# Performance work log

Measured on AMD Instinct MI355X. Metric: run time of the kernel, lower is better.

## Reference

```python
import jax, jax.numpy as jnp
import numpy as np

N, C, H, W = 512, 512, 7, 7
K = 64
ALPHA = 100.0
HW = H * W


def _up13(x):
    # bilinear upsample (..., 7, 7) -> (..., 13, 13), align_corners=True
    src = jnp.arange(13, dtype=jnp.float32) * (6.0 / 12.0)
    i0 = jnp.floor(src).astype(jnp.int32)
    i1 = jnp.minimum(i0 + 1, 6)
    w = src - i0.astype(jnp.float32)
    xr = x[..., i0, :] * (1.0 - w)[:, None] + x[..., i1, :] * w[:, None]  # rows
    xc = xr[..., :, i0] * (1.0 - w) + xr[..., :, i1] * w                  # cols
    return xc


def _conv2d(x, w, b, p):
    y = jax.lax.conv_general_dilated(
        x, w, window_strides=(1, 1), padding=[(p, p), (p, p)],
        dimension_numbers=('NCHW', 'OIHW', 'NCHW'))
    return y + b[None, :, None, None]


def setup_inputs() -> dict:
    key = jax.random.key(0)
    ks = jax.random.split(key, 16)
    x = jax.random.normal(ks[0], (N, C, H, W), jnp.float32)
    centroids = jax.random.uniform(ks[1], (K, C), jnp.float32)
    # conv params initialized from centroids as in _init_params (separate params after init)
    conv_w = 2.0 * ALPHA * centroids                    # (K, C) 1x1 conv kernel
    conv_b = -ALPHA * jnp.linalg.norm(centroids, axis=1)
    ln_w = jnp.ones((7, 7), jnp.float32)
    ln_b = jnp.zeros((7, 7), jnp.float32)
    c3_w = 0.02 * jax.random.normal(ks[2], (32, 512, 3, 3), jnp.float32)
    c3_b = jnp.zeros((32,), jnp.float32)
    c5_w = 0.02 * jax.random.normal(ks[3], (32, 512, 5, 5), jnp.float32)
    c5_b = jnp.zeros((32,), jnp.float32)
    c7_w = 0.02 * jax.random.normal(ks[4], (20, 512, 7, 7), jnp.float32)
    c7_b = jnp.zeros((20,), jnp.float32)
    dw_w = 0.1 * jax.random.normal(ks[5], (7, 13), jnp.float32)
    dw_b = jnp.zeros((7,), jnp.float32)
    dh_w = 0.1 * jax.random.normal(ks[6], (7, 13), jnp.float32)
    dh_b = jnp.zeros((7,), jnp.float32)
    acc_w = 0.1 * jax.random.normal(ks[7], (1, 84), jnp.float32)  # 1x1 conv (O, I)
    acc_b = jnp.zeros((1,), jnp.float32)
    return dict(x=x, centroids=centroids, conv_w=conv_w, conv_b=conv_b,
                ln_w=ln_w, ln_b=ln_b, c3_w=c3_w, c3_b=c3_b, c5_w=c5_w, c5_b=c5_b,
                c7_w=c7_w, c7_b=c7_b, dw_w=dw_w, dw_b=dw_b, dh_w=dh_w, dh_b=dh_b,
                acc_w=acc_w, acc_b=acc_b)


def reference(x, centroids, conv_w, conv_b, ln_w, ln_b,
              c3_w, c3_b, c5_w, c5_b, c7_w, c7_b,
              dw_w, dw_b, dh_w, dh_b, acc_w, acc_b):
    # ---- CRN on the raw (un-normalized) input ----
    mu = jnp.mean(x, axis=(-2, -1), keepdims=True)
    var = jnp.mean((x - mu) ** 2, axis=(-2, -1), keepdims=True)
    h = (x - mu) / jnp.sqrt(var + 1e-5) * ln_w + ln_b          # LayerNorm([7,7])
    h = _up13(h)                                               # (N,512,13,13)
    h = jnp.concatenate([_conv2d(h, c3_w, c3_b, 1),
                         _conv2d(h, c5_w, c5_b, 2),
                         _conv2d(h, c7_w, c7_b, 3)], axis=1)   # (N,84,13,13)
    h = jnp.einsum('nchw,ow->ncho', h, dw_w) + dw_b            # width 13->7
    h = h.transpose(0, 1, 3, 2)
    h = jnp.einsum('nchw,ow->ncho', h, dh_w) + dh_b            # height 13->7
    cw = jnp.einsum('nchw,oc->nohw', h, acc_w) + acc_b[None, :, None, None]
    cw = cw.reshape(N, 1, HW)                                  # context weights

    # ---- descriptor-wise L2 normalization over channels ----
    nrm = jnp.sqrt(jnp.sum(x * x, axis=1, keepdims=True))
    xn = x / jnp.maximum(nrm, 1e-12)

    # ---- soft assignment (1x1 conv + softmax over clusters) ----
    logits = (jnp.einsum('nchw,kc->nkhw', xn, conv_w)
              + conv_b[None, :, None, None]).reshape(N, K, HW)
    sa = jax.nn.softmax(logits, axis=1)
    mask = sa * cw                                             # (N,K,HW)

    # ---- fused VLAD aggregation (same math as masked residual sum) ----
    xf = xn.reshape(N, C, HW)
    vlad = jnp.einsum('nkl,ncl->nkc', mask, xf) \
        - centroids[None, :, :] * jnp.sum(mask, axis=-1)[:, :, None]
    vlad = vlad / jnp.maximum(jnp.linalg.norm(vlad, axis=2, keepdims=True), 1e-12)
    vlad = vlad.reshape(N, K * C)
    vlad = vlad / jnp.maximum(jnp.linalg.norm(vlad, axis=1, keepdims=True), 1e-12)
    return vlad
```

## Files before the change

kernel.cpp:

```cpp
#include <hip/hip_runtime.h>
#include <math.h>

#define NI 512
#define CC 512
#define KCL 64
#define HW49 49
#define CQ 25088
#define AP 260
#define GP 68
#define XQP 132

__device__ __forceinline__ float Uval(int i, int u) {
    if (i & 1) return (u == ((i - 1) >> 1) || u == ((i + 1) >> 1)) ? 0.5f : 0.0f;
    return (u == (i >> 1)) ? 1.0f : 0.0f;
}

__global__ __launch_bounds__(256) void kG(
    const float* __restrict__ c3w, const float* __restrict__ c5w, const float* __restrict__ c7w,
    const float* __restrict__ dww, const float* __restrict__ dhw, const float* __restrict__ accw,
    const float* __restrict__ lnw, const float* __restrict__ lnb,
    float* __restrict__ Gmat, float* __restrict__ Gl)
{
    const int c = blockIdx.x;
    const int t = threadIdx.x;
    __shared__ float dh[91], dw[91];
    __shared__ float Fh3[147], Fw3[147], Fh5[245], Fw5[245], Fh7[343], Fw7[343];
    __shared__ float wa3[9], wa5[25], wa7[49];
    __shared__ float Gtmp[2401];
    if (t < 91) dh[t] = dhw[t];
    if (t >= 128 && t < 219) dw[t - 128] = dww[t - 128];
    __syncthreads();
    for (int idx = t; idx < 147; idx += 256) {
        int oh = idx / 21, r = idx % 21, u = r / 3, dy = r % 3;
        float sh = 0.f, sw = 0.f;
        for (int i = 0; i < 13; i++) { int y = i - dy + 1; if (y >= 0 && y < 13) { float uu = Uval(i, u); sh += dh[oh * 13 + y] * uu; sw += dw[oh * 13 + y] * uu; } }
        Fh3[idx] = sh; Fw3[idx] = sw;
    }
    for (int idx = t; idx < 245; idx += 256) {
        int oh = idx / 35, r = idx % 35, u = r / 5, dy = r % 5;
        float sh = 0.f, sw = 0.f;
        for (int i = 0; i < 13; i++) { int y = i - dy + 2; if (y >= 0 && y < 13) { float uu = Uval(i, u); sh += dh[oh * 13 + y] * uu; sw += dw[oh * 13 + y] * uu; } }
        Fh5[idx] = sh; Fw5[idx] = sw;
    }
    for (int idx = t; idx < 343; idx += 256) {
        int oh = idx / 49, r = idx % 49, u = r / 7, dy = r % 7;
        float sh = 0.f, sw = 0.f;
        for (int i = 0; i < 13; i++) { int y = i - dy + 3; if (y >= 0 && y < 13) { float uu = Uval(i, u); sh += dh[oh * 13 + y] * uu; sw += dw[oh * 13 + y] * uu; } }
        Fh7[idx] = sh; Fw7[idx] = sw;
    }
    if (t < 9)               { float s = 0.f; for (int co = 0; co < 32; co++) s += accw[co]      * c3w[(size_t)(co * 512 + c) * 9  + t];        wa3[t] = s; }
    if (t >= 32 && t < 57)   { int q = t - 32; float s = 0.f; for (int co = 0; co < 32; co++) s += accw[32 + co] * c5w[(size_t)(co * 512 + c) * 25 + q]; wa5[q] = s; }
    if (t >= 64 && t < 113)  { int q = t - 64; float s = 0.f; for (int co = 0; co < 20; co++) s += accw[64 + co] * c7w[(size_t)(co * 512 + c) * 49 + q]; wa7[q] = s; }
    __syncthreads();
    for (int o = t; o < 2401; o += 256) {
        int q = o / 49, p = o % 49;
        int u = q / 7, v = q % 7, ow = p / 7, oh = p % 7;
        float acc = 0.f;
        #pragma unroll
        for (int dy = 0; dy < 3; dy++) { float fh = Fh3[(oh * 7 + u) * 3 + dy];
            #pragma unroll
            for (int dx = 0; dx < 3; dx++) acc += wa3[dy * 3 + dx] * fh * Fw3[(ow * 7 + v) * 3 + dx]; }
        #pragma unroll
        for (int dy = 0; dy < 5; dy++) { float fh = Fh5[(oh * 7 + u) * 5 + dy];
            #pragma unroll
            for (int dx = 0; dx < 5; dx++) acc += wa5[dy * 5 + dx] * fh * Fw5[(ow * 7 + v) * 5 + dx]; }
        #pragma unroll
        for (int dy = 0; dy < 7; dy++) { float fh = Fh7[(oh * 7 + u) * 7 + dy];
            #pragma unroll
            for (int dx = 0; dx < 7; dx++) acc += wa7[dy * 7 + dx] * fh * Fw7[(ow * 7 + v) * 7 + dx]; }
        Gtmp[o] = acc;
        Gmat[(size_t)c * 2401 + o] = acc * lnw[q];
    }
    __syncthreads();
    if (t < 49) {
        float s = 0.f;
        for (int q = 0; q < 49; q++) s += Gtmp[q * 49 + t] * lnb[q];
        Gl[c * 49 + t] = s;
    }
}

__global__ void kCb(const float* __restrict__ c3b, const float* __restrict__ c5b, const float* __restrict__ c7b,
                    const float* __restrict__ dww, const float* __restrict__ dwb,
                    const float* __restrict__ dhw, const float* __restrict__ dhb,
                    const float* __restrict__ accw, const float* __restrict__ accb,
                    const float* __restrict__ Gl, float* __restrict__ Cb)
{
    __shared__ float A0s, A1s, Sdw[7], Sdh[7];
    int t = threadIdx.x;
    if (t == 0) {
        float a0 = 0.f, a1 = 0.f;
        for (int co = 0; co < 84; co++) {
            float aw = accw[co]; a0 += aw;
            float b = (co < 32) ? c3b[co] : ((co < 64) ? c5b[co - 32] : c7b[co - 64]);
            a1 += aw * b;
        }
        A0s = a0; A1s = a1;
    }
    if (t < 7)             { float s = 0.f; for (int xx = 0; xx < 13; xx++) s += dww[t * 13 + xx]; Sdw[t] = s; }
    if (t >= 8 && t < 15)  { int oh = t - 8; float s = 0.f; for (int y = 0; y < 13; y++) s += dhw[oh * 13 + y]; Sdh[oh] = s; }
    __syncthreads();
    if (t < 49) {
        int ow = t / 7, oh = t % 7;
        float g = 0.f;
        for (int c = 0; c < 512; c++) g += Gl[c * 49 + t];
        Cb[t] = A1s * Sdw[ow] * Sdh[oh] + A0s * (dwb[ow] * Sdh[oh] + dhb[oh]) + accb[0] + g;
    }
}

__global__ __launch_bounds__(512) void kCw1(const float* __restrict__ x,
    const float* __restrict__ Gmat, float* __restrict__ part)
{
    __shared__ float As[49 * AP];
    __shared__ float Gs[49 * GP];
    const int b = blockIdx.x;
    const int nt = b >> 8, ks = b & 255;
    const int n0 = nt * 256;
    const int t = threadIdx.x;
    const int tn = t >> 3;
    const int tp = t & 7;
    float acc[4][8];
    #pragma unroll
    for (int j = 0; j < 4; j++)
        #pragma unroll
        for (int m = 0; m < 8; m++) acc[j][m] = 0.f;
    for (int kk = 0; kk < 2; kk++) {
        const int c = ks * 2 + kk;
        for (int i = t; i < 12544; i += 512) {
            int nr = i / 49, q = i - nr * 49;
            As[q * AP + nr] = x[(size_t)(n0 + nr) * CQ + (size_t)c * 49 + q];
        }
        for (int i = t; i < 2401; i += 512) {
            int q = i / 49, p = i - q * 49;
            Gs[q * GP + p] = Gmat[(size_t)c * 2401 + i];
        }
        for (int i = t; i < 735; i += 512) {
            int q = i / 15, pc = 49 + (i - q * 15);
            Gs[q * GP + pc] = 0.f;
        }
        __syncthreads();
        if (t < 256) {
            float s = 0.f, ss = 0.f;
            for (int q = 0; q < 49; q++) { float v = As[q * AP + t]; s += v; ss += v * v; }
            float mu = s * (1.f / 49.f);
            float var = ss * (1.f / 49.f) - mu * mu;
            float rs = 1.f / sqrtf(var + 1e-5f);
            for (int q = 0; q < 49; q++) As[q * AP + t] = (As[q * AP + t] - mu) * rs;
        }
        __syncthreads();
        for (int q = 0; q < 49; q++) {
            float4 a0 = *(const float4*)&As[q * AP + tn * 4];
            float4 g0 = *(const float4*)&Gs[q * GP + tp * 8];
            float4 g1 = *(const float4*)&Gs[q * GP + tp * 8 + 4];
            float av[4] = {a0.x, a0.y, a0.z, a0.w};
            float gv[8] = {g0.x, g0.y, g0.z, g0.w, g1.x, g1.y, g1.z, g1.w};
            #pragma unroll
            for (int j = 0; j < 4; j++)
                #pragma unroll
                for (int m = 0; m < 8; m++) acc[j][m] += av[j] * gv[m];
        }
        __syncthreads();
    }
    #pragma unroll
    for (int j = 0; j < 4; j++) {
        #pragma unroll
        for (int m = 0; m < 8; m++) {
            int p = tp * 8 + m;
            if (p < 49) As[(tn * 4 + j) * 49 + p] = acc[j][m];
        }
    }
    __syncthreads();
    {
        float* dst = part + (size_t)ks * CQ + (size_t)n0 * 49;
        for (int i = t; i < 12544; i += 512) dst[i] = As[i];
    }
}

__global__ __launch_bounds__(512) void kLog(const float* __restrict__ x,
    const float* __restrict__ convw, const float* __restrict__ convb,
    const float* __restrict__ part, const float* __restrict__ Cbg,
    float* __restrict__ maskr, float* __restrict__ msum)
{
    __shared__ float xq[2][49 * XQP];
    __shared__ float lg[64 * 52];
    __shared__ float ps[8 * 56];
    __shared__ float rn[49], cwl[49], smax[49], sinv[49];
    __shared__ float cb[64];
    __shared__ float pmx[392], psm[392];
    const int n = blockIdx.x;
    const int t = threadIdx.x;
    const int lane = t & 63;
    const int kw = __builtin_amdgcn_readfirstlane(t >> 6);
    const float* xp = x + (size_t)n * CQ;

    int scg[4], sl[4];
    #pragma unroll
    for (int s = 0; s < 4; s++) {
        int idx = t + s * 512;
        scg[s] = idx / 49; sl[s] = idx - scg[s] * 49;
    }
    float4 r[4];
    #pragma unroll
    for (int s = 0; s < 4; s++) {
        if (s < 3 || t < 32) {
            const float* src = xp + (size_t)(scg[s] * 4) * 49 + sl[s];
            r[s].x = src[0]; r[s].y = src[49]; r[s].z = src[98]; r[s].w = src[147];
        }
    }
    if (lane < 49) {
        const float* bp = part + (size_t)(kw * 32) * CQ + (size_t)n * 49 + lane;
        float s0 = 0.f, s1 = 0.f, s2 = 0.f, s3 = 0.f;
        for (int i = 0; i < 32; i += 4) {
            s0 += bp[(size_t)(i + 0) * CQ];
            s1 += bp[(size_t)(i + 1) * CQ];
            s2 += bp[(size_t)(i + 2) * CQ];
            s3 += bp[(size_t)(i + 3) * CQ];
        }
        psm[lane * 8 + kw] = (s0 + s1) + (s2 + s3);
    }
    if (t < 64) cb[t] = convb[t];

    float a[8] = {0.f, 0.f, 0.f, 0.f, 0.f, 0.f, 0.f, 0.f};
    float rs_part = 0.f;

    #pragma unroll
    for (int s = 0; s < 4; s++)
        if (s < 3 || t < 32) *(float4*)&xq[0][sl[s] * XQP + scg[s] * 4] = r[s];
    #pragma unroll
    for (int s = 0; s < 4; s++) {
        if (s < 3 || t < 32) {
            const float* src = xp + (size_t)(128 + scg[s] * 4) * 49 + sl[s];
            r[s].x = src[0]; r[s].y = src[49]; r[s].z = src[98]; r[s].w = src[147];
        }
    }
    __syncthreads();
    if (t < 49) {
        float s = Cbg[t];
        #pragma unroll
        for (int q = 0; q < 8; q++) s += psm[t * 8 + q];
        cwl[t] = s;
    }
    for (int qt = 0; qt < 4; qt++) {
        const float* buf = xq[qt & 1];
        if (lane < 49) {
            const float* row = &buf[lane * XQP + kw * 16];
            #pragma unroll
            for (int c4 = 0; c4 < 4; c4++) {
                float4 v = *(const float4*)(row + c4 * 4);
                rs_part += v.x * v.x + v.y * v.y + v.z * v.z + v.w * v.w;
            }
        }
        {
            const int lr = (lane < 49) ? lane : 48;
            const float* xrow = &buf[lr * XQP];
            const float* wb = convw + (size_t)(kw * 8) * 512 + qt * 128;
            for (int c4 = 0; c4 < 32; c4++) {
                float4 xv = *(const float4*)(xrow + c4 * 4);
                #pragma unroll
                for (int j = 0; j < 8; j++) {
                    float4 wv = *(const float4*)&wb[j * 512 + c4 * 4];
                    a[j] += wv.x * xv.x + wv.y * xv.y + wv.z * xv.z + wv.w * xv.w;
                }
            }
        }
        if (qt < 3) {
            #pragma unroll
            for (int s = 0; s < 4; s++)
                if (s < 3 || t < 32) *(float4*)&xq[(qt + 1) & 1][sl[s] * XQP + scg[s] * 4] = r[s];
            if (qt < 2) {
                #pragma unroll
                for (int s = 0; s < 4; s++) {
                    if (s < 3 || t < 32) {
                        const float* src = xp + (size_t)((qt + 2) * 128 + scg[s] * 4) * 49 + sl[s];
                        r[s].x = src[0]; r[s].y = src[49]; r[s].z = src[98]; r[s].w = src[147];
                    }
                }
            }
            __syncthreads();
        }
    }
    if (lane < 49) ps[kw * 56 + lane] = rs_part;
    __syncthreads();
    if (t < 49) {
        float s = 0.f;
        #pragma unroll
        for (int q = 0; q < 8; q++) s += ps[q * 56 + t];
        rn[t] = 1.f / fmaxf(sqrtf(s), 1e-12f);
    }
    __syncthreads();
    if (lane < 49) {
        float r0 = rn[lane];
        #pragma unroll
        for (int j = 0; j < 8; j++) lg[(kw * 8 + j) * 52 + lane] = a[j] * r0 + cb[kw * 8 + j];
    }
    __syncthreads();
    if (t < 392) {
        int l = t >> 3, kq = t & 7;
        float m = -3.402823466e38f;
        #pragma unroll
        for (int j = 0; j < 8; j++) m = fmaxf(m, lg[(kq * 8 + j) * 52 + l]);
        pmx[t] = m;
    }
    __syncthreads();
    if (t < 49) {
        float m = pmx[t * 8];
        #pragma unroll
        for (int q = 1; q < 8; q++) m = fmaxf(m, pmx[t * 8 + q]);
        smax[t] = m;
    }
    __syncthreads();
    if (t < 392) {
        int l = t >> 3, kq = t & 7;
        float m = smax[l], s = 0.f;
        #pragma unroll
        for (int j = 0; j < 8; j++) s += __expf(lg[(kq * 8 + j) * 52 + l] - m);
        psm[t] = s;
    }
    __syncthreads();
    if (t < 49) {
        float s = 0.f;
        #pragma unroll
        for (int q = 0; q < 8; q++) s += psm[t * 8 + q];
        sinv[t] = 1.f / s;
    }
    __syncthreads();
    if (t < 392) {
        int l = t >> 3, kq = t & 7;
        float m = smax[l], si = sinv[l] * cwl[l];
        #pragma unroll
        for (int j = 0; j < 8; j++) {
            int idx = (kq * 8 + j) * 52 + l;
            lg[idx] = __expf(lg[idx] - m) * si;
        }
    }
    __syncthreads();
    {
        float msr[8];
        #pragma unroll
        for (int j = 0; j < 8; j++) {
            float s = 0.f;
            for (int l = 0; l < 49; l++) s += lg[(kw * 8 + j) * 52 + l];
            msr[j] = s;
        }
        if (lane == 0) {
            #pragma unroll
            for (int j = 0; j < 8; j++) msum[n * 64 + kw * 8 + j] = msr[j];
        }
    }
    for (int o = t; o < 3136; o += 512) {
        int k = o / 49, l = o - k * 49;
        maskr[(size_t)n * 3136 + o] = lg[k * 52 + l] * rn[l];
    }
}

__global__ __launch_bounds__(512) void kVd(const float* __restrict__ x,
    const float* __restrict__ maskr, const float* __restrict__ msum,
    const float* __restrict__ cent, float* __restrict__ out)
{
    __shared__ float xh[12560];
    __shared__ float lg[64 * 52];
    __shared__ float ssq[64], scl[64];
    const int n = blockIdx.x;
    const int t = threadIdx.x;
    const int lane = t & 63;
    const int kw = __builtin_amdgcn_readfirstlane(t >> 6);
    const float* xp = x + (size_t)n * CQ;
    for (int i = t; i < 3136; i += 512) { int k = i / 49, l = i - k * 49; lg[k * 52 + l] = maskr[(size_t)n * 3136 + i]; }
    for (int i = t; i < 192; i += 512) { lg[(i / 3) * 52 + 49 + (i % 3)] = 0.f; }
    float msr[8];
    #pragma unroll
    for (int j = 0; j < 8; j++) msr[j] = msum[n * 64 + kw * 8 + j];
    float accA[8][4], accB[8][4];
    #pragma unroll
    for (int j = 0; j < 8; j++)
        #pragma unroll
        for (int ci = 0; ci < 4; ci++) { accA[j][ci] = 0.f; accB[j][ci] = 0.f; }
    for (int i4 = t; i4 < 3136; i4 += 512)
        *(float4*)&xh[i4 * 4] = *(const float4*)&xp[12544 + i4 * 4];
    if (t < 16) xh[12544 + t] = 0.f;
    __syncthreads();
    for (int lq = 0; lq < 13; lq++) {
        float xr[4][4];
        #pragma unroll
        for (int ci = 0; ci < 4; ci++)
            #pragma unroll
            for (int dl = 0; dl < 4; dl++)
                xr[ci][dl] = xh[(lane + 64 * ci) * 49 + lq * 4 + dl];
        #pragma unroll
        for (int j = 0; j < 8; j++) {
            float4 mv = *(const float4*)&lg[(kw * 8 + j) * 52 + lq * 4];
            #pragma unroll
            for (int ci = 0; ci < 4; ci++)
                accB[j][ci] += mv.x * xr[ci][0] + mv.y * xr[ci][1] + mv.z * xr[ci][2] + mv.w * xr[ci][3];
        }
    }
    __syncthreads();
    for (int i4 = t; i4 < 3136; i4 += 512)
        *(float4*)&xh[i4 * 4] = *(const float4*)&xp[i4 * 4];
    if (t < 16) xh[12544 + t] = 0.f;
    __syncthreads();
    for (int lq = 0; lq < 13; lq++) {
        float xr[4][4];
        #pragma unroll
        for (int ci = 0; ci < 4; ci++)
            #pragma unroll
            for (int dl = 0; dl < 4; dl++)
                xr[ci][dl] = xh[(lane + 64 * ci) * 49 + lq * 4 + dl];
        #pragma unroll
        for (int j = 0; j < 8; j++) {
            float4 mv = *(const float4*)&lg[(kw * 8 + j) * 52 + lq * 4];
            #pragma unroll
            for (int ci = 0; ci < 4; ci++)
                accA[j][ci] += mv.x * xr[ci][0] + mv.y * xr[ci][1] + mv.z * xr[ci][2] + mv.w * xr[ci][3];
        }
    }
    float ssr[8];
    #pragma unroll
    for (int j = 0; j < 8; j++) {
        int k = kw * 8 + j;
        float ms = msr[j];
        float s = 0.f;
        #pragma unroll
        for (int ci = 0; ci < 4; ci++) {
            int c = lane + 64 * ci;
            float va = accA[j][ci] - cent[(size_t)k * 512 + c] * ms;
            float vb = accB[j][ci] - cent[(size_t)k * 512 + 256 + c] * ms;
            accA[j][ci] = va; accB[j][ci] = vb;
            s += va * va + vb * vb;
        }
        ssr[j] = s;
    }
    #pragma unroll
    for (int j = 0; j < 8; j++)
        for (int off = 32; off >= 1; off >>= 1) ssr[j] += __shfl_xor(ssr[j], off, 64);
    if (lane == 0) {
        #pragma unroll
        for (int j = 0; j < 8; j++) ssq[kw * 8 + j] = ssr[j];
    }
    __syncthreads();
    if (t < 64) {
        float nrm = sqrtf(ssq[t]);
        float inv = 1.f / fmaxf(nrm, 1e-12f);
        float sk = nrm * inv;
        float g = sk * sk;
        #pragma unroll
        for (int off = 32; off >= 1; off >>= 1) g += __shfl_xor(g, off, 64);
        scl[t] = inv * (1.f / fmaxf(sqrtf(g), 1e-12f));
    }
    __syncthreads();
    #pragma unroll
    for (int j = 0; j < 8; j++) {
        int k = kw * 8 + j;
        float s2 = scl[k];
        #pragma unroll
        for (int ci = 0; ci < 4; ci++) {
            int c = lane + 64 * ci;
            out[(size_t)n * 32768 + (size_t)k * 512 + c] = accA[j][ci] * s2;
            out[(size_t)n * 32768 + (size_t)k * 512 + 256 + c] = accB[j][ci] * s2;
        }
    }
}

extern "C" void kernel_launch(void* const* d_in, const int* in_sizes, int n_in,
                              void* d_out, int out_size, void* d_ws, size_t ws_size,
                              hipStream_t stream)
{
    const float* x     = (const float*)d_in[0];
    const float* cent  = (const float*)d_in[1];
    const float* convw = (const float*)d_in[2];
    const float* convb = (const float*)d_in[3];
    const float* lnw   = (const float*)d_in[4];
    const float* lnb   = (const float*)d_in[5];
    const float* c3w   = (const float*)d_in[6];
    const float* c3b   = (const float*)d_in[7];
    const float* c5w   = (const float*)d_in[8];
    const float* c5b   = (const float*)d_in[9];
    const float* c7w   = (const float*)d_in[10];
    const float* c7b   = (const float*)d_in[11];
    const float* dww   = (const float*)d_in[12];
    const float* dwb   = (const float*)d_in[13];
    const float* dhw   = (const float*)d_in[14];
    const float* dhb   = (const float*)d_in[15];
    const float* accw  = (const float*)d_in[16];
    const float* accb  = (const float*)d_in[17];
    float* out = (float*)d_out;

    char* ws = (char*)d_ws;
    float* Gmat  = (float*)(ws);
    float* Gl    = (float*)(ws + 4917248);
    float* Cb    = (float*)(ws + 5017600);
    float* part  = (float*)(ws + 5017856);
    float* maskr = (float*)(ws + 30707968);
    float* msumW = (float*)(ws + 37130496);

    kG   <<<512, 256, 0, stream>>>(c3w, c5w, c7w, dww, dhw, accw, lnw, lnb, Gmat, Gl);
    kCb  <<<1,   64,  0, stream>>>(c3b, c5b, c7b, dww, dwb, dhw, dhb, accw, accb, Gl, Cb);
    kCw1 <<<512, 512, 0, stream>>>(x, Gmat, part);
    kLog <<<512, 512, 0, stream>>>(x, convw, convb, part, Cb, maskr, msumW);
    kVd  <<<512, 512, 0, stream>>>(x, maskr, msumW, cent, out);
}
```

Baseline: 180.9 us.

## Split logits kernel into channel-halved partial GEMM and separate softmax kernel

The fused logits/softmax kernel is split in two. The first kernel runs 1024 blocks, each computing partial logits and squared norms over half of the channels for one sample. The second kernel sums the two partials, normalizes, and does the softmax and masking. This doubles the block count to raise occupancy and shrinks shared memory per block, at the cost of an extra launch and a global round trip for the partial logits.

After: 283.4 us. 56.6% more time.

```diff
diff --git a/kernel.cpp b/kernel.cpp
--- a/kernel.cpp
+++ b/kernel.cpp
@@ -8,7 +8,7 @@
 #define CQ 25088
 #define AP 260
 #define GP 68
-#define XQP 132
+#define EP 68
 
 __device__ __forceinline__ float Uval(int i, int u) {
     if (i & 1) return (u == ((i - 1) >> 1) || u == ((i + 1) >> 1)) ? 0.5f : 0.0f;
@@ -175,14 +175,102 @@
     }
 }
 
-__global__ __launch_bounds__(512) void kLog(const float* __restrict__ x,
-    const float* __restrict__ convw, const float* __restrict__ convb,
-    const float* __restrict__ part, const float* __restrict__ Cbg,
-    float* __restrict__ maskr, float* __restrict__ msum)
-{
-    __shared__ float xq[2][49 * XQP];
+__global__ __launch_bounds__(512) void kLogA(const float* __restrict__ x,
+    const float* __restrict__ convw, float* __restrict__ lgP, float* __restrict__ rnP)
+{
+    __shared__ float xq[2][49 * EP];
+    __shared__ float ps[8 * 56];
+    const int b = blockIdx.x;
+    const int n = b >> 1, h = b & 1;
+    const int t = threadIdx.x;
+    const int lane = t & 63;
+    const int kw = __builtin_amdgcn_readfirstlane(t >> 6);
+    const float* xp = x + (size_t)n * CQ + (size_t)h * 12544;
+
+    int scg[2], sl[2];
+    #pragma unroll
+    for (int s = 0; s < 2; s++) { int idx = t + s * 512; scg[s] = idx / 49; sl[s] = idx - scg[s] * 49; }
+    const bool v1 = (t < 272);
+    float4 r[2];
+    #pragma unroll
+    for (int s = 0; s < 2; s++) {
+        if (s == 0 || v1) {
+            const float* src = xp + (size_t)(scg[s] * 4) * 49 + sl[s];
+            r[s].x = src[0]; r[s].y = src[49]; r[s].z = src[98]; r[s].w = src[147];
+        }
+    }
+    #pragma unroll
+    for (int s = 0; s < 2; s++)
+        if (s == 0 || v1) *(float4*)&xq[0][sl[s] * EP + scg[s] * 4] = r[s];
+    #pragma unroll
+    for (int s = 0; s < 2; s++) {
+        if (s == 0 || v1) {
+            const float* src = xp + 3136 + (size_t)(scg[s] * 4) * 49 + sl[s];
+            r[s].x = src[0]; r[s].y = src[49]; r[s].z = src[98]; r[s].w = src[147];
+        }
+    }
+    __syncthreads();
+
+    float a[8] = {0.f, 0.f, 0.f, 0.f, 0.f, 0.f, 0.f, 0.f};
+    float rs_part = 0.f;
+    for (int e = 0; e < 4; e++) {
+        const float* buf = xq[e & 1];
+        if (lane < 49) {
+            const float* row = &buf[lane * EP + kw * 8];
+            float4 v0 = *(const float4*)(row);
+            float4 v4 = *(const float4*)(row + 4);
+            rs_part += v0.x * v0.x + v0.y * v0.y + v0.z * v0.z + v0.w * v0.w
+                     + v4.x * v4.x + v4.y * v4.y + v4.z * v4.z + v4.w * v4.w;
+        }
+        {
+            const int lr = (lane < 49) ? lane : 48;
+            const float* xrow = &buf[lr * EP];
+            const float* wb = convw + (size_t)(kw * 8) * 512 + h * 256 + e * 64;
+            for (int c4 = 0; c4 < 16; c4++) {
+                float4 xv = *(const float4*)(xrow + c4 * 4);
+                #pragma unroll
+                for (int j = 0; j < 8; j++) {
+                    float4 wv = *(const float4*)&wb[(size_t)j * 512 + c4 * 4];
+                    a[j] += wv.x * xv.x + wv.y * xv.y + wv.z * xv.z + wv.w * xv.w;
+                }
+            }
+        }
+        if (e < 3) {
+            #pragma unroll
+            for (int s = 0; s < 2; s++)
+                if (s == 0 || v1) *(float4*)&xq[(e + 1) & 1][sl[s] * EP + scg[s] * 4] = r[s];
+            if (e < 2) {
+                #pragma unroll
+                for (int s = 0; s < 2; s++) {
+                    if (s == 0 || v1) {
+                        const float* src = xp + (size_t)(e + 2) * 3136 + (size_t)(scg[s] * 4) * 49 + sl[s];
+                        r[s].x = src[0]; r[s].y = src[49]; r[s].z = src[98]; r[s].w = src[147];
+                    }
+                }
+            }
+            __syncthreads();
+        }
+    }
+    if (lane < 49) ps[kw * 56 + lane] = rs_part;
+    __syncthreads();
+    if (t < 49) {
+        float s = 0.f;
+        #pragma unroll
+        for (int q = 0; q < 8; q++) s += ps[q * 56 + t];
+        rnP[(size_t)(n * 2 + h) * 49 + t] = s;
+    }
+    if (lane < 49) {
+        float* dst = lgP + (size_t)(n * 2 + h) * 3136;
+        #pragma unroll
+        for (int j = 0; j < 8; j++) dst[(kw * 8 + j) * 49 + lane] = a[j];
+    }
+}
+
+__global__ __launch_bounds__(512) void kSoft(const float* __restrict__ lgP,
+    const float* __restrict__ rnP, const float* __restrict__ part, const float* __restrict__ Cbg,
+    const float* __restrict__ convb, float* __restrict__ maskr, float* __restrict__ msum)
+{
     __shared__ float lg[64 * 52];
-    __shared__ float ps[8 * 56];
     __shared__ float rn[49], cwl[49], smax[49], sinv[49];
     __shared__ float cb[64];
     __shared__ float pmx[392], psm[392];
@@ -190,22 +278,7 @@
     const int t = threadIdx.x;
     const int lane = t & 63;
     const int kw = __builtin_amdgcn_readfirstlane(t >> 6);
-    const float* xp = x + (size_t)n * CQ;
-
-    int scg[4], sl[4];
-    #pragma unroll
-    for (int s = 0; s < 4; s++) {
-        int idx = t + s * 512;
-        scg[s] = idx / 49; sl[s] = idx - scg[s] * 49;
-    }
-    float4 r[4];
-    #pragma unroll
-    for (int s = 0; s < 4; s++) {
-        if (s < 3 || t < 32) {
-            const float* src = xp + (size_t)(scg[s] * 4) * 49 + sl[s];
-            r[s].x = src[0]; r[s].y = src[49]; r[s].z = src[98]; r[s].w = src[147];
-        }
-    }
+
     if (lane < 49) {
         const float* bp = part + (size_t)(kw * 32) * CQ + (size_t)n * 49 + lane;
         float s0 = 0.f, s1 = 0.f, s2 = 0.f, s3 = 0.f;
@@ -217,20 +290,11 @@
         }
         psm[lane * 8 + kw] = (s0 + s1) + (s2 + s3);
     }
-    if (t < 64) cb[t] = convb[t];
-
-    float a[8] = {0.f, 0.f, 0.f, 0.f, 0.f, 0.f, 0.f, 0.f};
-    float rs_part = 0.f;
-
-    #pragma unroll
-    for (int s = 0; s < 4; s++)
-        if (s < 3 || t < 32) *(float4*)&xq[0][sl[s] * XQP + scg[s] * 4] = r[s];
-    #pragma unroll
-    for (int s = 0; s < 4; s++) {
-        if (s < 3 || t < 32) {
-            const float* src = xp + (size_t)(128 + scg[s] * 4) * 49 + sl[s];
-            r[s].x = src[0]; r[s].y = src[49]; r[s].z = src[98]; r[s].w = src[147];
-        }
+    if (t >= 448) cb[t - 448] = convb[t - 448];
+    if (t >= 64 && t < 113) {
+        int l = t - 64;
+        float rs = rnP[(size_t)(n * 2) * 49 + l] + rnP[(size_t)(n * 2 + 1) * 49 + l];
+        rn[l] = 1.f / fmaxf(sqrtf(rs), 1e-12f);
     }
     __syncthreads();
     if (t < 49) {
@@ -239,58 +303,13 @@
         for (int q = 0; q < 8; q++) s += psm[t * 8 + q];
         cwl[t] = s;
     }
-    for (int qt = 0; qt < 4; qt++) {
-        const float* buf = xq[qt & 1];
-        if (lane < 49) {
-            const float* row = &buf[lane * XQP + kw * 16];
-            #pragma unroll
-            for (int c4 = 0; c4 < 4; c4++) {
-                float4 v = *(const float4*)(row + c4 * 4);
-                rs_part += v.x * v.x + v.y * v.y + v.z * v.z + v.w * v.w;
-            }
-        }
-        {
-            const int lr = (lane < 49) ? lane : 48;
-            const float* xrow = &buf[lr * XQP];
-            const float* wb = convw + (size_t)(kw * 8) * 512 + qt * 128;
-            for (int c4 = 0; c4 < 32; c4++) {
-                float4 xv = *(const float4*)(xrow + c4 * 4);
-                #pragma unroll
-                for (int j = 0; j < 8; j++) {
-                    float4 wv = *(const float4*)&wb[j * 512 + c4 * 4];
-                    a[j] += wv.x * xv.x + wv.y * xv.y + wv.z * xv.z + wv.w * xv.w;
-                }
-            }
-        }
-        if (qt < 3) {
-            #pragma unroll
-            for (int s = 0; s < 4; s++)
-                if (s < 3 || t < 32) *(float4*)&xq[(qt + 1) & 1][sl[s] * XQP + scg[s] * 4] = r[s];
-            if (qt < 2) {
-                #pragma unroll
-                for (int s = 0; s < 4; s++) {
-                    if (s < 3 || t < 32) {
-                        const float* src = xp + (size_t)((qt + 2) * 128 + scg[s] * 4) * 49 + sl[s];
-                        r[s].x = src[0]; r[s].y = src[49]; r[s].z = src[98]; r[s].w = src[147];
-                    }
-                }
-            }
-            __syncthreads();
-        }
-    }
-    if (lane < 49) ps[kw * 56 + lane] = rs_part;
-    __syncthreads();
-    if (t < 49) {
-        float s = 0.f;
-        #pragma unroll
-        for (int q = 0; q < 8; q++) s += ps[q * 56 + t];
-        rn[t] = 1.f / fmaxf(sqrtf(s), 1e-12f);
-    }
-    __syncthreads();
-    if (lane < 49) {
-        float r0 = rn[lane];
-        #pragma unroll
-        for (int j = 0; j < 8; j++) lg[(kw * 8 + j) * 52 + lane] = a[j] * r0 + cb[kw * 8 + j];
+    {
+        const float* pA = lgP + (size_t)(n * 2) * 3136;
+        const float* pB = lgP + (size_t)(n * 2 + 1) * 3136;
+        for (int o = t; o < 3136; o += 512) {
+            int k = o / 49, l = o - k * 49;
+            lg[k * 52 + l] = (pA[o] + pB[o]) * rn[l] + cb[k];
+        }
     }
     __syncthreads();
     if (t < 392) {
@@ -491,10 +510,13 @@
     float* part  = (float*)(ws + 5017856);
     float* maskr = (float*)(ws + 30707968);
     float* msumW = (float*)(ws + 37130496);
-
-    kG   <<<512, 256, 0, stream>>>(c3w, c5w, c7w, dww, dhw, accw, lnw, lnb, Gmat, Gl);
-    kCb  <<<1,   64,  0, stream>>>(c3b, c5b, c7b, dww, dwb, dhw, dhb, accw, accb, Gl, Cb);
-    kCw1 <<<512, 512, 0, stream>>>(x, Gmat, part);
-    kLog <<<512, 512, 0, stream>>>(x, convw, convb, part, Cb, maskr, msumW);
-    kVd  <<<512, 512, 0, stream>>>(x, maskr, msumW, cent, out);
-}
+    float* lgP   = (float*)(ws + 37261568);
+    float* rnP   = (float*)(ws + 50106624);
+
+    kG    <<<512,  256, 0, stream>>>(c3w, c5w, c7w, dww, dhw, accw, lnw, lnb, Gmat, Gl);
+    kCb   <<<1,    64,  0, stream>>>(c3b, c5b, c7b, dww, dwb, dhw, dhb, accw, accb, Gl, Cb);
+    kCw1  <<<512,  512, 0, stream>>>(x, Gmat, part);
+    kLogA <<<1024, 512, 0, stream>>>(x, convw, lgP, rnP);
+    kSoft <<<512,  512, 0, stream>>>(lgP, rnP, part, Cb, convb, maskr, msumW);
+    kVd   <<<512,  512, 0, stream>>>(x, maskr, msumW, cent, out);
+}
```
